# Kernel optimization log

Measured on AMD Instinct MI355X. Metric: run time of the kernel, lower is better.

The kernel has to match this reference:

```python
import jax, jax.numpy as jnp
import numpy as np

NUM_EXPERTS = 64
TOP_K = 2
NOISE_STD = 0.1


def setup_inputs() -> dict:
    key = jax.random.key(0)
    k1, k2, k3 = jax.random.split(key, 3)
    x = jax.random.normal(k1, (8192, 4096), dtype=jnp.float32)
    W = jax.random.normal(k2, (NUM_EXPERTS, 4096), dtype=jnp.float32) * 0.01  # nn.init.normal_(std=0.01)
    noise = jax.random.normal(k3, (8192, NUM_EXPERTS), dtype=jnp.float32)
    return {"x": x, "W": W, "noise": noise}


def reference(x, W, noise):
    batch = x.shape[0]
    # router_logits = x @ W^T  -> [batch, num_experts]
    router_logits = jnp.einsum("bd,ed->be", x, W)
    noisy_logits = router_logits + NOISE_STD * noise  # training=True path
    top_k_logits, top_k_indices = jax.lax.top_k(noisy_logits, TOP_K)
    expert_weights = jax.nn.softmax(top_k_logits, axis=-1)
    # load balancing loss (Switch Transformer): one_hot(sel).sum over k and batch
    # replaced by scatter-add counts per expert
    counts = jnp.zeros((NUM_EXPERTS,), dtype=jnp.float32).at[top_k_indices.reshape(-1)].add(1.0)
    fraction_tokens = counts / batch
    router_probs = jax.nn.softmax(router_logits, axis=-1)
    mean_router_prob = router_probs.mean(axis=0)
    load_balance_loss = NUM_EXPERTS * jnp.sum(fraction_tokens * mean_router_prob)
    return (top_k_indices, expert_weights, router_logits, load_balance_loss)
```

## Files before the change

kernel.cpp:

```cpp
#include <hip/hip_runtime.h>
#include <hip/hip_bf16.h>

#define BATCH 8192
#define DMODEL 4096
#define NEXP 64

typedef __attribute__((ext_vector_type(8))) short short8;
typedef __attribute__((ext_vector_type(4))) float f32x4;

#define WF_FLOATS  393216

#define GLD16(dst_lds, src_g)                                                  \
    __builtin_amdgcn_global_load_lds(                                          \
        (const __attribute__((address_space(1))) void*)(src_g),                \
        (__attribute__((address_space(3))) void*)(dst_lds), 16, 0, 0)

__global__ __launch_bounds__(256) void build_wf(const float* __restrict__ W,
                                                unsigned short* __restrict__ WF2,
                                                float* __restrict__ zbase)
{
    const int t = threadIdx.x;
    if (blockIdx.x == 0) {
        zbase[t] = 0.f;
        zbase[t + 256] = 0.f;
    }

    const int gid = blockIdx.x * 256 + t;
    const int ks = gid >> 8;
    const int cf = (gid >> 6) & 3;
    const int l  = gid & 63;
    const int e  = cf * 16 + (l & 15);
    const int k0 = ks * 32 + (l >> 4) * 8;
    const float* src = W + (size_t)e * DMODEL + k0;

    short8 hv, mv, lv;
#pragma unroll
    for (int j = 0; j < 8; ++j) {
        const float xv = src[j];
        const __hip_bfloat16 h = __float2bfloat16(xv);
        const float r1 = xv - __bfloat162float(h);
        const __hip_bfloat16 m = __float2bfloat16(r1);
        const float r2 = r1 - __bfloat162float(m);
        const __hip_bfloat16 lo = __float2bfloat16(r2);
        hv[j] = (short)__builtin_bit_cast(unsigned short, h);
        mv[j] = (short)__builtin_bit_cast(unsigned short, m);
        lv[j] = (short)__builtin_bit_cast(unsigned short, lo);
    }
    const size_t base = (size_t)ks * 6144 + cf * 512 + l * 8;
    *(short8*)&WF2[base]        = hv;
    *(short8*)&WF2[base + 2048] = mv;
    *(short8*)&WF2[base + 4096] = lv;
}


#define CVT1(V, J, AH, AM, AL) {                                              \
    const float xv_ = (V);                                                    \
    const __hip_bfloat16 h_ = __float2bfloat16(xv_);                          \
    const float r1_ = xv_ - __bfloat162float(h_);                             \
    const __hip_bfloat16 m_ = __float2bfloat16(r1_);                          \
    const float r2_ = r1_ - __bfloat162float(m_);                             \
    const __hip_bfloat16 l_ = __float2bfloat16(r2_);                          \
    AH[J] = (short)__builtin_bit_cast(unsigned short, h_);                    \
    AM[J] = (short)__builtin_bit_cast(unsigned short, m_);                    \
    AL[J] = (short)__builtin_bit_cast(unsigned short, l_); }

#define CVT8(X0, X1, AH, AM, AL)                                              \
    CVT1(X0[0], 0, AH, AM, AL) CVT1(X0[1], 1, AH, AM, AL)                     \
    CVT1(X0[2], 2, AH, AM, AL) CVT1(X0[3], 3, AH, AM, AL)                     \
    CVT1(X1[0], 4, AH, AM, AL) CVT1(X1[1], 5, AH, AM, AL)                     \
    CVT1(X1[2], 6, AH, AM, AL) CVT1(X1[3], 7, AH, AM, AL)

#define MFMA(A, B, C) __builtin_amdgcn_mfma_f32_16x16x32_bf16(A, B, C, 0, 0, 0)

__global__ __launch_bounds__(256, 4) void gemm_mfma(const float* __restrict__ x,
                                                    const unsigned short* __restrict__ WF2,
                                                    float* __restrict__ part,
                                                    int S)
{
    __shared__ float xs[2][2048];
    __shared__ unsigned short wsh[2][6144];

    const int t = threadIdx.x;
    const int l = t & 63;
    const int wid = t >> 6;
    const int g = blockIdx.x & 127;
    const int s = blockIdx.x >> 7;
    const int rowbase = g * 64;
    const int kbeg = s * (DMODEL / S);
    const int nsteps = (DMODEL / S) >> 5;

    const float* pxa[2];
#pragma unroll
    for (int r = 0; r < 2; ++r) {
        const int tr = wid * 16 + r * 8 + (l >> 3);
        const int ul = (l & 7) ^ (tr & 7);
        pxa[r] = x + (size_t)(rowbase + tr) * DMODEL + kbeg + ul * 4;
    }
    const unsigned short* pwb = WF2 + (size_t)(kbeg >> 5) * 6144 + t * 8;

#define STAGE(BUF, IT) {                                                       \
    _Pragma("unroll")                                                          \
    for (int r_ = 0; r_ < 2; ++r_)                                             \
        GLD16(&xs[BUF][wid * 512 + r_ * 256], pxa[r_] + (size_t)(IT) * 32);    \
    _Pragma("unroll")                                                          \
    for (int r_ = 0; r_ < 3; ++r_)                                             \
        GLD16(&wsh[BUF][r_ * 2048 + wid * 512],                                \
              pwb + (size_t)(IT) * 6144 + r_ * 2048); }

    const int lr = l & 15;
    const int lk = l >> 4;
    const int xr = lr & 7;
    const int trw = wid * 16 + lr;
    const int a0 = trw * 32 + (((lk * 2)     ^ xr) * 4);
    const int a1 = trw * 32 + (((lk * 2 + 1) ^ xr) * 4);

    f32x4 acc[4] = {};

    STAGE(0, 0)

    for (int it = 0; it < nsteps; ++it) {
        const int cur = it & 1;
        if (it + 1 < nsteps) {
            STAGE(cur ^ 1, it + 1)
            asm volatile("s_waitcnt vmcnt(5)" ::: "memory");
        } else {
            asm volatile("s_waitcnt vmcnt(0)" ::: "memory");
        }
        __builtin_amdgcn_s_barrier();

        const f32x4 xa0 = *(const f32x4*)&xs[cur][a0];
        const f32x4 xa1 = *(const f32x4*)&xs[cur][a1];
        short8 ah, am, al;
        CVT8(xa0, xa1, ah, am, al)

#pragma unroll
        for (int cf = 0; cf < 4; ++cf) {
            const unsigned short* wp = &wsh[cur][cf * 512 + l * 8];
            const short8 bh = *(const short8*)(wp);
            const short8 bm = *(const short8*)(wp + 2048);
            const short8 bl = *(const short8*)(wp + 4096);
            acc[cf] = MFMA(ah, bh, acc[cf]);
            acc[cf] = MFMA(ah, bm, acc[cf]);
            acc[cf] = MFMA(am, bh, acc[cf]);
            acc[cf] = MFMA(ah, bl, acc[cf]);
            acc[cf] = MFMA(al, bh, acc[cf]);
            acc[cf] = MFMA(am, bm, acc[cf]);
        }
        __builtin_amdgcn_s_barrier();
    }

    const int orow = lk * 4;
#pragma unroll
    for (int j = 0; j < 4; ++j) {
        const int row = rowbase + wid * 16 + orow + j;
        float* dst = part + ((size_t)s * BATCH + row) * NEXP + lr;
#pragma unroll
        for (int cf = 0; cf < 4; ++cf)
            dst[cf * 16] = acc[cf][j];
    }
#undef STAGE
}

template<int NS>
__global__ __launch_bounds__(256) void router2(const float* __restrict__ part,
                                               const float* __restrict__ noise,
                                               float* __restrict__ out,
                                               float* __restrict__ probsum,
                                               float* __restrict__ counts,
                                               int* __restrict__ done)
{
    __shared__ float sps[4][64];
    __shared__ float scnt[4][64];
    __shared__ int lastFlag;

    const int t = threadIdx.x;
    const int w = t >> 6;
    const int lane = t & 63;
    const int wg = blockIdx.x * 4 + w;

    float* out_idx = out;
    float* out_w = out + 16384;
    float* out_logits = out + 32768;

    float psum_local = 0.f;
    float cnt_local = 0.f;

    for (int r = 0; r < 8; ++r) {
        const int row = wg * 8 + r;
        float lgt = 0.f;
#pragma unroll
        for (int s = 0; s < NS; ++s)
            lgt += part[((size_t)s * BATCH + row) * NEXP + lane];
        out_logits[(size_t)row * NEXP + lane] = lgt;

        const float ny = lgt + 0.1f * noise[(size_t)row * NEXP + lane];

        float v1 = ny; int i1 = lane;
#pragma unroll
        for (int m = 32; m >= 1; m >>= 1) {
            float ov = __shfl_xor(v1, m);
            int oi = __shfl_xor(i1, m);
            if (ov > v1 || (ov == v1 && oi < i1)) { v1 = ov; i1 = oi; }
        }
        float v2 = (lane == i1) ? -1e30f : ny; int i2 = lane;
#pragma unroll
        for (int m = 32; m >= 1; m >>= 1) {
            float ov = __shfl_xor(v2, m);
            int oi = __shfl_xor(i2, m);
            if (ov > v2 || (ov == v2 && oi < i2)) { v2 = ov; i2 = oi; }
        }

        if (lane == 0) {
            const float d = expf(v2 - v1);
            const float w1 = 1.0f / (1.0f + d);
            out_idx[row * 2 + 0] = (float)i1;
            out_idx[row * 2 + 1] = (float)i2;
            out_w[row * 2 + 0] = w1;
            out_w[row * 2 + 1] = 1.0f - w1;
        }

        float m = lgt;
#pragma unroll
        for (int ss = 32; ss >= 1; ss >>= 1) m = fmaxf(m, __shfl_xor(m, ss));
        const float p = expf(lgt - m);
        float sum = p;
#pragma unroll
        for (int ss = 32; ss >= 1; ss >>= 1) sum += __shfl_xor(sum, ss);
        psum_local += p / sum;
        cnt_local += (lane == i1 ? 1.f : 0.f) + (lane == i2 ? 1.f : 0.f);
    }

    sps[w][lane] = psum_local;
    scnt[w][lane] = cnt_local;
    __syncthreads();
    if (t < 64) {
        float ssum = 0.f, c = 0.f;
#pragma unroll
        for (int ww = 0; ww < 4; ++ww) { ssum += sps[ww][t]; c += scnt[ww][t]; }
        atomicAdd(&probsum[t], ssum);
        atomicAdd(&counts[t], c);
    }
    __syncthreads();
    if (t == 0) {
        __threadfence();
        lastFlag = (atomicAdd(done, 1) == (int)gridDim.x - 1) ? 1 : 0;
    }
    __syncthreads();
    if (lastFlag && t < 64) {
        const float ps = __hip_atomic_load(&probsum[t], __ATOMIC_RELAXED,
                                           __HIP_MEMORY_SCOPE_AGENT);
        const float ct = __hip_atomic_load(&counts[t], __ATOMIC_RELAXED,
                                           __HIP_MEMORY_SCOPE_AGENT);
        float v = ps * ct;
#pragma unroll
        for (int ss = 32; ss >= 1; ss >>= 1) v += __shfl_xor(v, ss);
        if (t == 0)
            out[557056] = (float)NEXP * v / ((float)BATCH * (float)BATCH);
    }
}

extern "C" void kernel_launch(void* const* d_in, const int* in_sizes, int n_in,
                              void* d_out, int out_size, void* d_ws, size_t ws_size,
                              hipStream_t stream)
{
    const float* x = (const float*)d_in[0];
    const float* W = (const float*)d_in[1];
    const float* noise = (const float*)d_in[2];
    float* out = (float*)d_out;
    float* ws = (float*)d_ws;

    float* probsum = ws;
    float* counts = ws + 64;
    int* done = (int*)(ws + 128);
    unsigned short* WF2 = (unsigned short*)(ws + 512);
    float* part = ws + 512 + WF_FLOATS;

    int S = 1;
    const size_t base_floats = 512 + WF_FLOATS;
    for (int cand = 8; cand >= 1; cand >>= 1) {
        const size_t need = (base_floats + (size_t)cand * BATCH * NEXP) * sizeof(float);
        if (ws_size >= need) { S = cand; break; }
    }

    build_wf<<<128, 256, 0, stream>>>(W, WF2, ws);
    gemm_mfma<<<128 * S, 256, 0, stream>>>(x, WF2, part, S);
    switch (S) {
        case 8: router2<8><<<256, 256, 0, stream>>>(part, noise, out, probsum, counts, done); break;
        case 4: router2<4><<<256, 256, 0, stream>>>(part, noise, out, probsum, counts, done); break;
        case 2: router2<2><<<256, 256, 0, stream>>>(part, noise, out, probsum, counts, done); break;
        default: router2<1><<<256, 256, 0, stream>>>(part, noise, out, probsum, counts, done); break;
    }
}
```

Measured before the change: 62.73 us.

## Replace 3-way bf16 split GEMM with scaled 2-way fp16 split

Splits x and W into fp16 high and scaled-residual low parts instead of three bf16 pieces. This cuts the per-step MFMA count from six to three and shrinks the W staging buffer and its global loads by a third. W is prescaled by 64 and residuals by 2048, and the two accumulators are recombined with the inverse scales at store time. This risks fp16 range overflow for large x values and a different precision profile than the bf16x3 scheme.

```diff
diff --git a/kernel.cpp b/kernel.cpp
--- a/kernel.cpp
+++ b/kernel.cpp
@@ -8,7 +8,7 @@
 typedef __attribute__((ext_vector_type(8))) short short8;
 typedef __attribute__((ext_vector_type(4))) float f32x4;
 
-#define WF_FLOATS  393216
+#define WF_FLOATS  262144
 
 #define GLD16(dst_lds, src_g)                                                  \
     __builtin_amdgcn_global_load_lds(                                          \
@@ -33,44 +33,37 @@
     const int k0 = ks * 32 + (l >> 4) * 8;
     const float* src = W + (size_t)e * DMODEL + k0;
 
-    short8 hv, mv, lv;
+    short8 hv, lv;
 #pragma unroll
     for (int j = 0; j < 8; ++j) {
-        const float xv = src[j];
-        const __hip_bfloat16 h = __float2bfloat16(xv);
-        const float r1 = xv - __bfloat162float(h);
-        const __hip_bfloat16 m = __float2bfloat16(r1);
-        const float r2 = r1 - __bfloat162float(m);
-        const __hip_bfloat16 lo = __float2bfloat16(r2);
+        const float wv = src[j] * 64.0f;
+        const _Float16 h = (_Float16)wv;
+        const float r = (wv - (float)h) * 2048.0f;
+        const _Float16 lo = (_Float16)r;
         hv[j] = (short)__builtin_bit_cast(unsigned short, h);
-        mv[j] = (short)__builtin_bit_cast(unsigned short, m);
         lv[j] = (short)__builtin_bit_cast(unsigned short, lo);
     }
-    const size_t base = (size_t)ks * 6144 + cf * 512 + l * 8;
+    const size_t base = (size_t)ks * 4096 + cf * 512 + l * 8;
     *(short8*)&WF2[base]        = hv;
-    *(short8*)&WF2[base + 2048] = mv;
-    *(short8*)&WF2[base + 4096] = lv;
-}
-
-
-#define CVT1(V, J, AH, AM, AL) {                                              \
+    *(short8*)&WF2[base + 2048] = lv;
+}
+
+
+#define CVTF1(V, J, AH, AL) {                                                 \
     const float xv_ = (V);                                                    \
-    const __hip_bfloat16 h_ = __float2bfloat16(xv_);                          \
-    const float r1_ = xv_ - __bfloat162float(h_);                             \
-    const __hip_bfloat16 m_ = __float2bfloat16(r1_);                          \
-    const float r2_ = r1_ - __bfloat162float(m_);                             \
-    const __hip_bfloat16 l_ = __float2bfloat16(r2_);                          \
+    const _Float16 h_ = (_Float16)xv_;                                        \
+    const float r_ = (xv_ - (float)h_) * 2048.0f;                             \
+    const _Float16 l_ = (_Float16)r_;                                         \
     AH[J] = (short)__builtin_bit_cast(unsigned short, h_);                    \
-    AM[J] = (short)__builtin_bit_cast(unsigned short, m_);                    \
     AL[J] = (short)__builtin_bit_cast(unsigned short, l_); }
 
-#define CVT8(X0, X1, AH, AM, AL)                                              \
-    CVT1(X0[0], 0, AH, AM, AL) CVT1(X0[1], 1, AH, AM, AL)                     \
-    CVT1(X0[2], 2, AH, AM, AL) CVT1(X0[3], 3, AH, AM, AL)                     \
-    CVT1(X1[0], 4, AH, AM, AL) CVT1(X1[1], 5, AH, AM, AL)                     \
-    CVT1(X1[2], 6, AH, AM, AL) CVT1(X1[3], 7, AH, AM, AL)
-
-#define MFMA(A, B, C) __builtin_amdgcn_mfma_f32_16x16x32_bf16(A, B, C, 0, 0, 0)
+#define CVTF8(X0, X1, AH, AL)                                                 \
+    CVTF1(X0[0], 0, AH, AL) CVTF1(X0[1], 1, AH, AL)                           \
+    CVTF1(X0[2], 2, AH, AL) CVTF1(X0[3], 3, AH, AL)                           \
+    CVTF1(X1[0], 4, AH, AL) CVTF1(X1[1], 5, AH, AL)                           \
+    CVTF1(X1[2], 6, AH, AL) CVTF1(X1[3], 7, AH, AL)
+
+#define MFMAH(A, B, C) __builtin_amdgcn_mfma_f32_16x16x32_f16(A, B, C, 0, 0, 0)
 
 __global__ __launch_bounds__(256, 4) void gemm_mfma(const float* __restrict__ x,
                                                     const unsigned short* __restrict__ WF2,
@@ -78,7 +71,7 @@
                                                     int S)
 {
     __shared__ float xs[2][2048];
-    __shared__ unsigned short wsh[2][6144];
+    __shared__ unsigned short wsh[2][4096];
 
     const int t = threadIdx.x;
     const int l = t & 63;
@@ -96,16 +89,16 @@
         const int ul = (l & 7) ^ (tr & 7);
         pxa[r] = x + (size_t)(rowbase + tr) * DMODEL + kbeg + ul * 4;
     }
-    const unsigned short* pwb = WF2 + (size_t)(kbeg >> 5) * 6144 + t * 8;
+    const unsigned short* pwb = WF2 + (size_t)(kbeg >> 5) * 4096 + t * 8;
 
 #define STAGE(BUF, IT) {                                                       \
     _Pragma("unroll")                                                          \
     for (int r_ = 0; r_ < 2; ++r_)                                             \
         GLD16(&xs[BUF][wid * 512 + r_ * 256], pxa[r_] + (size_t)(IT) * 32);    \
     _Pragma("unroll")                                                          \
-    for (int r_ = 0; r_ < 3; ++r_)                                             \
+    for (int r_ = 0; r_ < 2; ++r_)                                             \
         GLD16(&wsh[BUF][r_ * 2048 + wid * 512],                                \
-              pwb + (size_t)(IT) * 6144 + r_ * 2048); }
+              pwb + (size_t)(IT) * 4096 + r_ * 2048); }
 
     const int lr = l & 15;
     const int lk = l >> 4;
@@ -114,7 +107,8 @@
     const int a0 = trw * 32 + (((lk * 2)     ^ xr) * 4);
     const int a1 = trw * 32 + (((lk * 2 + 1) ^ xr) * 4);
 
-    f32x4 acc[4] = {};
+    f32x4 acc0[4] = {};
+    f32x4 acc1[4] = {};
 
     STAGE(0, 0)
 
@@ -122,7 +116,7 @@
         const int cur = it & 1;
         if (it + 1 < nsteps) {
             STAGE(cur ^ 1, it + 1)
-            asm volatile("s_waitcnt vmcnt(5)" ::: "memory");
+            asm volatile("s_waitcnt vmcnt(4)" ::: "memory");
         } else {
             asm volatile("s_waitcnt vmcnt(0)" ::: "memory");
         }
@@ -130,21 +124,17 @@
 
         const f32x4 xa0 = *(const f32x4*)&xs[cur][a0];
         const f32x4 xa1 = *(const f32x4*)&xs[cur][a1];
-        short8 ah, am, al;
-        CVT8(xa0, xa1, ah, am, al)
+        short8 ah, al;
+        CVTF8(xa0, xa1, ah, al)
 
 #pragma unroll
         for (int cf = 0; cf < 4; ++cf) {
             const unsigned short* wp = &wsh[cur][cf * 512 + l * 8];
             const short8 bh = *(const short8*)(wp);
-            const short8 bm = *(const short8*)(wp + 2048);
-            const short8 bl = *(const short8*)(wp + 4096);
-            acc[cf] = MFMA(ah, bh, acc[cf]);
-            acc[cf] = MFMA(ah, bm, acc[cf]);
-            acc[cf] = MFMA(am, bh, acc[cf]);
-            acc[cf] = MFMA(ah, bl, acc[cf]);
-            acc[cf] = MFMA(al, bh, acc[cf]);
-            acc[cf] = MFMA(am, bm, acc[cf]);
+            const short8 bl = *(const short8*)(wp + 2048);
+            acc0[cf] = MFMAH(ah, bh, acc0[cf]);
+            acc1[cf] = MFMAH(ah, bl, acc1[cf]);
+            acc1[cf] = MFMAH(al, bh, acc1[cf]);
         }
         __builtin_amdgcn_s_barrier();
     }
@@ -156,7 +146,7 @@
         float* dst = part + ((size_t)s * BATCH + row) * NEXP + lr;
 #pragma unroll
         for (int cf = 0; cf < 4; ++cf)
-            dst[cf * 16] = acc[cf][j];
+            dst[cf * 16] = (acc0[cf][j] + acc1[cf][j] * 4.8828125e-4f) * 0.015625f;
     }
 #undef STAGE
 }
```

Result: faster. 58.07 us (median of 2 runs) (-7.4%).
